# Kernel tuning notes

Measured on AMD Instinct MI355X. Metric: run time of the kernel, lower is better.

The kernel has to match this reference:

```python
import jax, jax.numpy as jnp
import numpy as np

HEADS = 4
DIM_HEAD = 32


def setup_inputs() -> dict:
    key = jax.random.key(0)
    k1, k2, k3, k4 = jax.random.split(key, 4)
    x = jax.random.normal(k1, (2, 64, 48, 48, 48), dtype=jnp.float32)
    # 1x1x1 conv weights collapse to plain channel-mixing matrices
    w_qkv = jax.random.normal(k2, (384, 64), dtype=jnp.float32) * 0.05  # [3*heads*dh, dim]
    w_out = jax.random.normal(k3, (64, 128), dtype=jnp.float32) * 0.05  # [dim, heads*dh]
    b_out = jax.random.normal(k4, (64,), dtype=jnp.float32) * 0.05
    return {"x": x, "w_qkv": w_qkv, "w_out": w_out, "b_out": b_out}


def reference(x, w_qkv, w_out, b_out):
    b, c, D, H, W = x.shape
    N = D * H * W
    x_flat = x.reshape(b, c, N)
    # 1x1 conv == channel matmul: [b, 3*heads*dh, N]
    qkv = jnp.einsum('oc,bcn->bon', w_qkv, x_flat)
    # channel order: (qkv, heads, dh)
    qkv = qkv.reshape(b, 3, HEADS, DIM_HEAD, N)
    q, k, v = qkv[:, 0], qkv[:, 1], qkv[:, 2]
    k = jax.nn.softmax(k, axis=-1)  # softmax over the token axis N
    context = jnp.einsum('bhdn,bhen->bhde', k, v)   # [b, h, dh, dh]
    out = jnp.einsum('bhde,bhdn->bhen', context, q)  # [b, h, dh, N]
    out = out.reshape(b, HEADS * DIM_HEAD, N)
    y = jnp.einsum('oc,bcn->bon', w_out, out) + b_out[None, :, None]
    return y.reshape(b, c, D, H, W)
```

## Files before the change

kernel.cpp:

```cpp
#include <hip/hip_runtime.h>
#include <hip/hip_bf16.h>


#define C_IN 64

typedef __attribute__((ext_vector_type(8))) short short8;
typedef __attribute__((ext_vector_type(4))) float f32x4;

static __device__ __forceinline__ unsigned short f2bf(float f) {
    union { float f; unsigned u; } x; x.f = f;
    return (unsigned short)((x.u + 0x7fffu + ((x.u >> 16) & 1u)) >> 16);
}

static __device__ __forceinline__ unsigned cvt_pk_bf16(float lo, float hi) {
    __hip_bfloat162 h = __float22bfloat162_rn(float2{lo, hi});
    union { __hip_bfloat162 h; unsigned u; } cv;
    cv.h = h;
    return cv.u;
}

static __device__ __forceinline__ void lds_barrier() {
    __builtin_amdgcn_sched_barrier(0);
    asm volatile("s_waitcnt lgkmcnt(0)" ::: "memory");
    __builtin_amdgcn_s_barrier();
    __builtin_amdgcn_sched_barrier(0);
}

__global__ __launch_bounds__(256, 2)
void kv_ctx_fused(const float* __restrict__ x,
                  const float* __restrict__ w_qkv,
                  unsigned short* __restrict__ xT,
                  float* __restrict__ part,
                  int N, int nblk, int bbase)
{
    __shared__ __align__(16) unsigned short Xsb[64][68];
    __shared__ __align__(16) unsigned short Xbf[64][72];
    __shared__ __align__(16) char PVs[4 * 2 * 32 * 80];

    const int by  = blockIdx.y;
    const int b   = by + bbase;
    const int bx  = blockIdx.x;
    const int t   = threadIdx.x;
    const int w   = t >> 6;
    const int l   = t & 63;
    const int l15 = l & 15;
    const int lg  = l >> 4;

    const float* xb = x + (size_t)b * C_IN * N;
    const int n_blk = bx * 256;

    auto pv_ptr = [&](int p, int row, int colbf) -> unsigned short* {
        return (unsigned short*)(PVs + ((size_t)((w * 2 + p) * 32 + row) * 80
                                        + colbf * 2));
    };

    short8 Wfr[4][2];
    #pragma unroll
    for (int nt = 0; nt < 4; ++nt) {
        const int row = (nt < 2) ? (128 + w * 32 + nt * 16 + l15)
                                 : (256 + w * 32 + (nt - 2) * 16 + l15);
        const float* wr = w_qkv + (size_t)row * C_IN;
        #pragma unroll
        for (int s = 0; s < 2; ++s) {
            #pragma unroll
            for (int j = 0; j < 8; ++j)
                Wfr[nt][s][j] = (short)f2bf(wr[s * 32 + lg * 8 + j]);
        }
    }

    f32x4 acc2[2][2];
    #pragma unroll
    for (int dt = 0; dt < 2; ++dt)
        #pragma unroll
        for (int et = 0; et < 2; ++et)
            acc2[dt][et] = (f32x4){0.f, 0.f, 0.f, 0.f};
    float s_loc[2] = {0.f, 0.f};

    float4 ld0, ld1, ld2, ld3;

    #define ISSUE_LOADS(IT) {                                              \
        const int nb2 = n_blk + (IT) * 64;                                 \
        int slot, c, nq;                                                   \
        slot = 0 * 256 + t; c = slot >> 4; nq = slot & 15;                 \
        ld0 = *(const float4*)(xb + (size_t)c * N + nb2 + nq * 4);         \
        slot = 1 * 256 + t; c = slot >> 4; nq = slot & 15;                 \
        ld1 = *(const float4*)(xb + (size_t)c * N + nb2 + nq * 4);         \
        slot = 2 * 256 + t; c = slot >> 4; nq = slot & 15;                 \
        ld2 = *(const float4*)(xb + (size_t)c * N + nb2 + nq * 4);         \
        slot = 3 * 256 + t; c = slot >> 4; nq = slot & 15;                 \
        ld3 = *(const float4*)(xb + (size_t)c * N + nb2 + nq * 4);         \
    }
    #define STORE_XSB() {                                                  \
        float4 lds_[4] = {ld0, ld1, ld2, ld3};                             \
        _Pragma("unroll")                                                  \
        for (int i = 0; i < 4; ++i) {                                      \
            int slot = i * 256 + t;                                        \
            int c = slot >> 4, n4 = (slot & 15) * 4;                       \
            uint2 p;                                                       \
            p.x = cvt_pk_bf16(lds_[i].x, lds_[i].y);                       \
            p.y = cvt_pk_bf16(lds_[i].z, lds_[i].w);                       \
            *(uint2*)&Xsb[c][n4] = p;                                      \
        }                                                                  \
    }

    ISSUE_LOADS(0)
    STORE_XSB()
    lds_barrier();

    for (int it = 0; it < 4; ++it) {
        if (it < 3) ISSUE_LOADS(it + 1)

        {
            const int an = l;
            unsigned rowu[8];
            #pragma unroll
            for (int i = 0; i < 8; ++i) {
                unsigned lo = Xsb[w * 16 + 2 * i][an];
                unsigned hi = Xsb[w * 16 + 2 * i + 1][an];
                rowu[i] = lo | (hi << 16);
            }
            *(uint4*)&Xbf[an][w * 16]     = *(uint4*)&rowu[0];
            *(uint4*)&Xbf[an][w * 16 + 8] = *(uint4*)&rowu[4];
            unsigned short* dst = xT + ((size_t)by * N + n_blk + it * 64 + an) * 64 + w * 16;
            *(uint4*)(dst)     = *(uint4*)&rowu[0];
            *(uint4*)(dst + 8) = *(uint4*)&rowu[4];
        }
        lds_barrier();

        short8 Af[4][2];
        #pragma unroll
        for (int mt = 0; mt < 4; ++mt)
            #pragma unroll
            for (int s = 0; s < 2; ++s)
                Af[mt][s] = *(const short8*)&Xbf[mt * 16 + l15][s * 32 + lg * 8];

        #pragma unroll
        for (int h = 0; h < 2; ++h) {
            #pragma unroll
            for (int m2 = 0; m2 < 2; ++m2) {
                const int mt = h * 2 + m2;
                #pragma unroll
                for (int nt = 0; nt < 4; ++nt) {
                    f32x4 a = (f32x4){0.f, 0.f, 0.f, 0.f};
                    a = __builtin_amdgcn_mfma_f32_16x16x32_bf16(Af[mt][0], Wfr[nt][0], a, 0, 0, 0);
                    a = __builtin_amdgcn_mfma_f32_16x16x32_bf16(Af[mt][1], Wfr[nt][1], a, 0, 0, 0);
                    const int nh = m2 * 16 + lg * 4;
                    if (nt < 2) {
                        float e0 = __expf(a[0]), e1 = __expf(a[1]);
                        float e2 = __expf(a[2]), e3 = __expf(a[3]);
                        s_loc[nt] += (e0 + e1) + (e2 + e3);
                        uint2 p;
                        p.x = cvt_pk_bf16(e0, e1);
                        p.y = cvt_pk_bf16(e2, e3);
                        *(uint2*)pv_ptr(0, nt * 16 + l15, nh) = p;
                    } else {
                        uint2 p;
                        p.x = cvt_pk_bf16(a[0], a[1]);
                        p.y = cvt_pk_bf16(a[2], a[3]);
                        *(uint2*)pv_ptr(1, (nt - 2) * 16 + l15, nh) = p;
                    }
                }
            }
            {
                short8 A2[2], B2[2];
                #pragma unroll
                for (int dt = 0; dt < 2; ++dt)
                    A2[dt] = *(const short8*)pv_ptr(0, dt * 16 + l15, lg * 8);
                #pragma unroll
                for (int et = 0; et < 2; ++et)
                    B2[et] = *(const short8*)pv_ptr(1, et * 16 + l15, lg * 8);
                #pragma unroll
                for (int dt = 0; dt < 2; ++dt)
                    #pragma unroll
                    for (int et = 0; et < 2; ++et)
                        acc2[dt][et] = __builtin_amdgcn_mfma_f32_16x16x32_bf16(
                            A2[dt], B2[et], acc2[dt][et], 0, 0, 0);
            }
        }

        if (it < 3) STORE_XSB()
        lds_barrier();
    }
    #undef ISSUE_LOADS
    #undef STORE_XSB

    float* pb = part + ((size_t)b * nblk + bx) * 4224;
    #pragma unroll
    for (int dt = 0; dt < 2; ++dt)
        #pragma unroll
        for (int et = 0; et < 2; ++et)
            #pragma unroll
            for (int r = 0; r < 4; ++r)
                pb[(w * 32 + dt * 16 + lg * 4 + r) * 32 + et * 16 + l15] =
                    acc2[dt][et][r];

    #pragma unroll
    for (int nt = 0; nt < 2; ++nt) {
        float s = s_loc[nt];
        s += __shfl_xor(s, 16);
        s += __shfl_xor(s, 32);
        if (lg == 0)
            pb[4096 + w * 32 + nt * 16 + l15] = s;
    }
}

__global__ __launch_bounds__(256)
void reduce_kernel(const float* __restrict__ part,
                   float* __restrict__ part2,
                   int nblk)
{
    const int b  = blockIdx.z;
    const int cy = blockIdx.y;
    const int g  = blockIdx.x * 256 + threadIdx.x;
    if (g >= 4224) return;

    const int cnt = (nblk + 15) / 16;
    const int c0  = cy * cnt;
    const int c1  = (c0 + cnt < nblk) ? (c0 + cnt) : nblk;

    const float* pb = part + (size_t)b * nblk * 4224 + g;
    float a0 = 0.f, a1 = 0.f, a2 = 0.f, a3 = 0.f;
    int c = c0;
    for (; c + 4 <= c1; c += 4) {
        a0 += pb[(size_t)(c + 0) * 4224];
        a1 += pb[(size_t)(c + 1) * 4224];
        a2 += pb[(size_t)(c + 2) * 4224];
        a3 += pb[(size_t)(c + 3) * 4224];
    }
    for (; c < c1; ++c) a0 += pb[(size_t)c * 4224];
    part2[((size_t)b * 16 + cy) * 4224 + g] = (a0 + a1) + (a2 + a3);
}

__global__ __launch_bounds__(256)
void finalize_kernel(const float* __restrict__ part2,
                     const float* __restrict__ w_qkv,
                     const float* __restrict__ w_out,
                     unsigned short* __restrict__ wf_bf)
{
    const int b = blockIdx.y;
    const int s = blockIdx.x;
    const int t = threadIdx.x;

    __shared__ float Wq[128][64];
    __shared__ float Ctx[128][36];
    __shared__ float Tt[128][68];
    __shared__ float WoS[8][128];
    __shared__ float Sinv[128];

    #pragma unroll
    for (int i = 0; i < 8; ++i) {
        int idx = i * 1024 + t * 4;
        *(float4*)&Wq[idx >> 6][idx & 63] = *(const float4*)(w_qkv + idx);
    }
    {
        int idx = t * 4;
        int o = idx >> 7, he = idx & 127;
        *(float4*)&WoS[o][he] = *(const float4*)(w_out + (size_t)(s * 8 + o) * 128 + he);
    }
    if (t < 128) {
        float ssum = 0.f;
        #pragma unroll
        for (int rep = 0; rep < 16; ++rep)
            ssum += part2[((size_t)b * 16 + rep) * 4224 + 4096 + t];
        Sinv[t] = 1.0f / ssum;
    }
    float cacc[16];
    #pragma unroll
    for (int i = 0; i < 16; ++i) cacc[i] = 0.f;
    {
        const float* cb = part2 + (size_t)b * 16 * 4224;
        for (int rep = 0; rep < 16; ++rep) {
            #pragma unroll
            for (int i = 0; i < 16; ++i)
                cacc[i] += cb[(size_t)rep * 4224 + i * 256 + t];
        }
    }
    __syncthreads();

    #pragma unroll
    for (int i = 0; i < 16; ++i) {
        int idx = i * 256 + t;
        Ctx[idx >> 5][idx & 31] = cacc[i] * Sinv[idx >> 5];
    }
    __syncthreads();

    {
        const int he0 = (t >> 3) * 4;
        const int c0  = (t & 7) * 8;
        const int hh  = he0 >> 5;
        const int e0  = he0 & 31;
        float acc[4][8];
        #pragma unroll
        for (int j = 0; j < 4; ++j)
            #pragma unroll
            for (int k = 0; k < 8; ++k) acc[j][k] = 0.f;

        for (int d = 0; d < 32; ++d) {
            float4 cv = *(const float4*)&Ctx[hh * 32 + d][e0];
            float4 w0 = *(const float4*)&Wq[hh * 32 + d][c0];
            float4 w1 = *(const float4*)&Wq[hh * 32 + d][c0 + 4];
            float wv[8] = {w0.x, w0.y, w0.z, w0.w, w1.x, w1.y, w1.z, w1.w};
            float cvv[4] = {cv.x, cv.y, cv.z, cv.w};
            #pragma unroll
            for (int j = 0; j < 4; ++j)
                #pragma unroll
                for (int k = 0; k < 8; ++k)
                    acc[j][k] = fmaf(cvv[j], wv[k], acc[j][k]);
        }
        #pragma unroll
        for (int j = 0; j < 4; ++j) {
            *(float4*)&Tt[he0 + j][c0]     = make_float4(acc[j][0], acc[j][1], acc[j][2], acc[j][3]);
            *(float4*)&Tt[he0 + j][c0 + 4] = make_float4(acc[j][4], acc[j][5], acc[j][6], acc[j][7]);
        }
    }
    __syncthreads();

    {
        const int o = t >> 5;
        const int c = (t & 31) * 2;
        float a0 = 0.f, a1 = 0.f, b0 = 0.f, b1 = 0.f;
        #pragma unroll
        for (int he = 0; he < 128; he += 2) {
            float w0 = WoS[o][he], w1 = WoS[o][he + 1];
            float2 t0 = *(const float2*)&Tt[he][c];
            float2 t1 = *(const float2*)&Tt[he + 1][c];
            a0 = fmaf(w0, t0.x, a0); a1 = fmaf(w0, t0.y, a1);
            b0 = fmaf(w1, t1.x, b0); b1 = fmaf(w1, t1.y, b1);
        }
        unsigned short* dst = wf_bf + (size_t)b * 4096 + (size_t)(s * 8 + o) * 64 + c;
        dst[0] = f2bf(a0 + b0);
        dst[1] = f2bf(a1 + b1);
    }
}

__global__ __launch_bounds__(256)
void out_gemm_mfma(const unsigned short* __restrict__ xT,
                   const unsigned short* __restrict__ wf_bf,
                   const float* __restrict__ b_out,
                   float* __restrict__ y,
                   int N, int bbase)
{
    const int by  = blockIdx.y;
    const int b   = by + bbase;
    const int t   = threadIdx.x;
    const int w   = t >> 6;
    const int l   = t & 63;
    const int l15 = l & 15;
    const int lg  = l >> 4;
    const int nb  = blockIdx.x * 256 + w * 64;

    short8 Bf[4][2];
    const unsigned short* wb = wf_bf + (size_t)b * 4096;
    #pragma unroll
    for (int ot = 0; ot < 4; ++ot)
        #pragma unroll
        for (int s = 0; s < 2; ++s)
            Bf[ot][s] = *(const short8*)(wb + (size_t)(ot * 16 + l15) * 64
                                         + s * 32 + lg * 8);
    float bias[4];
    #pragma unroll
    for (int ot = 0; ot < 4; ++ot) bias[ot] = b_out[ot * 16 + l15];

    short8 Af[4][2];
    const unsigned short* xr = xT + ((size_t)by * N + nb) * 64;
    #pragma unroll
    for (int mt = 0; mt < 4; ++mt)
        #pragma unroll
        for (int s = 0; s < 2; ++s)
            Af[mt][s] = *(const short8*)(xr + (size_t)(mt * 16 + l15) * 64
                                         + s * 32 + lg * 8);

    float* yb = y + (size_t)b * C_IN * N;
    #pragma unroll
    for (int mt = 0; mt < 4; ++mt) {
        #pragma unroll
        for (int ot = 0; ot < 4; ++ot) {
            f32x4 a = (f32x4){0.f, 0.f, 0.f, 0.f};
            a = __builtin_amdgcn_mfma_f32_16x16x32_bf16(Af[mt][0], Bf[ot][0], a, 0, 0, 0);
            a = __builtin_amdgcn_mfma_f32_16x16x32_bf16(Af[mt][1], Bf[ot][1], a, 0, 0, 0);
            float4 v = make_float4(a[0] + bias[ot], a[1] + bias[ot],
                                   a[2] + bias[ot], a[3] + bias[ot]);
            *(float4*)(yb + (size_t)(ot * 16 + l15) * N + nb + mt * 16 + lg * 4) = v;
        }
    }
}

__global__ __launch_bounds__(256)
void transpose_kernel(const float* __restrict__ x,
                      unsigned short* __restrict__ xT,
                      int N, int bbase)
{
    __shared__ float Xs[64][65];
    const int b  = blockIdx.y + bbase;
    const int t  = threadIdx.x;
    const int n0 = blockIdx.x * 64;

    const float* xb = x + (size_t)b * C_IN * N;
    #pragma unroll
    for (int i = 0; i < 4; ++i) {
        int slot = i * 256 + t;
        int c = slot >> 4, nq = slot & 15;
        float4 v = *(const float4*)(xb + (size_t)c * N + n0 + nq * 4);
        Xs[c][nq * 4 + 0] = v.x; Xs[c][nq * 4 + 1] = v.y;
        Xs[c][nq * 4 + 2] = v.z; Xs[c][nq * 4 + 3] = v.w;
    }
    __syncthreads();

    const int n = t >> 2, q = t & 3;
    unsigned out[8];
    #pragma unroll
    for (int i = 0; i < 8; ++i)
        out[i] = cvt_pk_bf16(Xs[q * 16 + 2 * i][n], Xs[q * 16 + 2 * i + 1][n]);
    unsigned short* dst = xT + ((size_t)blockIdx.y * N + n0 + n) * 64 + q * 16;
    *(uint4*)(dst)     = *(uint4*)&out[0];
    *(uint4*)(dst + 8) = *(uint4*)&out[4];
}

extern "C" void kernel_launch(void* const* d_in, const int* in_sizes, int n_in,
                              void* d_out, int out_size, void* d_ws, size_t ws_size,
                              hipStream_t stream)
{
    const float* x     = (const float*)d_in[0];
    const float* w_qkv = (const float*)d_in[1];
    const float* w_out = (const float*)d_in[2];
    const float* b_out = (const float*)d_in[3];
    float* y = (float*)d_out;

    const int B = 2;
    const int N = in_sizes[0] / (B * C_IN);
    const int nblk = N / 256;

    const size_t xT_batch = (size_t)N * 64 * 2;
    const size_t part_b   = (size_t)B * nblk * 4224 * 4;
    const size_t p2_b     = (size_t)B * 16 * 4224 * 4;
    const size_t wf_b     = (size_t)B * 4096 * 2;
    const bool   full     = ws_size >= (size_t)B * xT_batch + part_b + p2_b + wf_b;

    unsigned short* xT    = (unsigned short*)d_ws;
    char* p               = (char*)d_ws + (full ? B * xT_batch : xT_batch);
    float* part           = (float*)p;
    float* part2          = part + (size_t)B * nblk * 4224;
    unsigned short* wf_bf = (unsigned short*)(part2 + (size_t)B * 16 * 4224);

    if (full) {
        kv_ctx_fused<<<dim3(nblk, B), 256, 0, stream>>>(x, w_qkv, xT, part, N, nblk, 0);
        reduce_kernel<<<dim3(17, 16, B), 256, 0, stream>>>(part, part2, nblk);
        finalize_kernel<<<dim3(8, B), 256, 0, stream>>>(part2, w_qkv, w_out, wf_bf);
        out_gemm_mfma<<<dim3(nblk, B), 256, 0, stream>>>(xT, wf_bf, b_out, y, N, 0);
    } else {
        for (int b = 0; b < B; ++b)
            kv_ctx_fused<<<dim3(nblk, 1), 256, 0, stream>>>(x, w_qkv, xT, part, N, nblk, b);
        reduce_kernel<<<dim3(17, 16, B), 256, 0, stream>>>(part, part2, nblk);
        finalize_kernel<<<dim3(8, B), 256, 0, stream>>>(part2, w_qkv, w_out, wf_bf);
        for (int b = 0; b < B; ++b) {
            transpose_kernel<<<dim3(N / 64, 1), 256, 0, stream>>>(x, xT, N, b);
            out_gemm_mfma<<<dim3(nblk, 1), 256, 0, stream>>>(xT, wf_bf, b_out, y, N, b);
        }
    }
}
```

Measured before the change: 66.31 us.

## Store x tile directly transposed into swizzled double-buffered LDS, drop transpose barrier

Converts the fp32 x tile to bf16 and writes it straight into an XOR-swizzled, token-major LDS buffer. This removes the separate channel-major staging buffer, the in-LDS transpose pass and one barrier per iteration. The buffer is double-buffered so the next tile can be stored while the current one is being read. The cost is scalar 2-byte LDS stores (16 per thread) in place of packed 8-byte stores, which may add LDS instruction pressure and bank conflicts.

```diff
diff --git a/kernel.cpp b/kernel.cpp
--- a/kernel.cpp
+++ b/kernel.cpp
@@ -24,6 +24,10 @@
     asm volatile("s_waitcnt lgkmcnt(0)" ::: "memory");
     __builtin_amdgcn_s_barrier();
     __builtin_amdgcn_sched_barrier(0);
+}
+
+static __device__ __forceinline__ int xbf_swz(int row) {
+    return ((row >> 2) & 7) << 4;
 }
 
 __global__ __launch_bounds__(256, 2)
@@ -33,8 +37,7 @@
                   float* __restrict__ part,
                   int N, int nblk, int bbase)
 {
-    __shared__ __align__(16) unsigned short Xsb[64][68];
-    __shared__ __align__(16) unsigned short Xbf[64][72];
+    __shared__ __align__(16) unsigned short Xbf[2][64][72];
     __shared__ __align__(16) char PVs[4 * 2 * 32 * 80];
 
     const int by  = blockIdx.y;
@@ -90,49 +93,52 @@
         slot = 3 * 256 + t; c = slot >> 4; nq = slot & 15;                 \
         ld3 = *(const float4*)(xb + (size_t)c * N + nb2 + nq * 4);         \
     }
-    #define STORE_XSB() {                                                  \
+    #define STORE_XBF(BUF) {                                               \
         float4 lds_[4] = {ld0, ld1, ld2, ld3};                             \
         _Pragma("unroll")                                                  \
         for (int i = 0; i < 4; ++i) {                                      \
             int slot = i * 256 + t;                                        \
-            int c = slot >> 4, n4 = (slot & 15) * 4;                       \
-            uint2 p;                                                       \
-            p.x = cvt_pk_bf16(lds_[i].x, lds_[i].y);                       \
-            p.y = cvt_pk_bf16(lds_[i].z, lds_[i].w);                       \
-            *(uint2*)&Xsb[c][n4] = p;                                      \
+            int c = slot >> 4, nq4 = (slot & 15) * 4;                      \
+            float v[4] = {lds_[i].x, lds_[i].y, lds_[i].z, lds_[i].w};     \
+            _Pragma("unroll")                                              \
+            for (int j = 0; j < 4; ++j) {                                  \
+                int row = nq4 + j;                                         \
+                int byte = (c * 2) ^ xbf_swz(row);                         \
+                *(unsigned short*)((char*)&Xbf[BUF][row][0] + byte) = f2bf(v[j]); \
+            }                                                              \
         }                                                                  \
     }
 
     ISSUE_LOADS(0)
-    STORE_XSB()
+    STORE_XBF(0)
     lds_barrier();
 
+    #pragma unroll
     for (int it = 0; it < 4; ++it) {
+        const int cur = it & 1;
         if (it < 3) ISSUE_LOADS(it + 1)
 
         {
             const int an = l;
-            unsigned rowu[8];
-            #pragma unroll
-            for (int i = 0; i < 8; ++i) {
-                unsigned lo = Xsb[w * 16 + 2 * i][an];
-                unsigned hi = Xsb[w * 16 + 2 * i + 1][an];
-                rowu[i] = lo | (hi << 16);
-            }
-            *(uint4*)&Xbf[an][w * 16]     = *(uint4*)&rowu[0];
-            *(uint4*)&Xbf[an][w * 16 + 8] = *(uint4*)&rowu[4];
+            const int swz = xbf_swz(an);
+            const char* rb = (const char*)&Xbf[cur][an][0];
+            uint4 r0 = *(const uint4*)(rb + ((w * 32) ^ swz));
+            uint4 r1 = *(const uint4*)(rb + ((w * 32 + 16) ^ swz));
             unsigned short* dst = xT + ((size_t)by * N + n_blk + it * 64 + an) * 64 + w * 16;
-            *(uint4*)(dst)     = *(uint4*)&rowu[0];
-            *(uint4*)(dst + 8) = *(uint4*)&rowu[4];
-        }
-        lds_barrier();
+            *(uint4*)(dst)     = r0;
+            *(uint4*)(dst + 8) = r1;
+        }
 
         short8 Af[4][2];
         #pragma unroll
-        for (int mt = 0; mt < 4; ++mt)
+        for (int mt = 0; mt < 4; ++mt) {
+            const int row = mt * 16 + l15;
+            const int swz = xbf_swz(row);
+            const char* rb = (const char*)&Xbf[cur][row][0];
             #pragma unroll
             for (int s = 0; s < 2; ++s)
-                Af[mt][s] = *(const short8*)&Xbf[mt * 16 + l15][s * 32 + lg * 8];
+                Af[mt][s] = *(const short8*)(rb + ((s * 64 + lg * 16) ^ swz));
+        }
 
         #pragma unroll
         for (int h = 0; h < 2; ++h) {
@@ -178,11 +184,11 @@
             }
         }
 
-        if (it < 3) STORE_XSB()
+        if (it < 3) STORE_XBF(cur ^ 1)
         lds_barrier();
     }
     #undef ISSUE_LOADS
-    #undef STORE_XSB
+    #undef STORE_XBF
 
     float* pb = part + ((size_t)b * nblk + bx) * 4224;
     #pragma unroll
```

After: 66.82 us. About the same (+0.8%).
